# Kernel tuning notes

Hardware: AMD Instinct MI355X
Metric: run time of the kernel (lower is better)

The kernel has to match this reference:

```python
import jax, jax.numpy as jnp
import numpy as np

B, S, E, H = 2, 2048, 512, 8
D = E // H  # head_dim = 64


def setup_inputs() -> dict:
    key = jax.random.key(0)
    ks = jax.random.split(key, 10)
    sc = 1.0 / np.sqrt(E)
    x = jax.random.normal(ks[0], (B, S, E), dtype=jnp.float32)
    # parent index per node: tree_structure[b][parent[b,i]] contains i
    parent = jax.random.randint(ks[1], (B, S), 0, S, dtype=jnp.int32)
    Wp = jax.random.normal(ks[2], (E, E), dtype=jnp.float32) * sc
    bp = jnp.zeros((E,), dtype=jnp.float32)
    Wc = jax.random.normal(ks[3], (E, E), dtype=jnp.float32) * sc
    bc = jnp.zeros((E,), dtype=jnp.float32)
    Ws = jax.random.normal(ks[4], (E, E), dtype=jnp.float32) * sc
    bs = jnp.zeros((E,), dtype=jnp.float32)
    Wo = jax.random.normal(ks[5], (E, E), dtype=jnp.float32) * sc
    bo = jnp.zeros((E,), dtype=jnp.float32)
    return {"x": x, "parent": parent, "Wp": Wp, "bp": bp, "Wc": Wc,
            "bc": bc, "Ws": Ws, "bs": bs, "Wo": Wo, "bo": bo}


def _tree_mask(parent):
    # Vectorized equivalent of the per-batch scatter loop:
    # mask[b, p, c] = mask[b, c, p] = 1 for each (parent, child) edge.
    b_idx = jnp.arange(B)[:, None]
    rows = jnp.arange(S)[None, :]
    m = jnp.zeros((B, S, S), dtype=bool)
    m = m.at[b_idx, rows, parent].set(True)
    m = m.at[b_idx, parent, rows].set(True)
    return m  # (B, S, S), broadcast over heads


def reference(x, parent, Wp, bp, Wc, bc, Ws, bs, Wo, bo):
    # Tri-projection
    p = (x @ Wp + bp).reshape(B, S, H, D)
    c = (x @ Wc + bc).reshape(B, S, H, D)
    s = (x @ Ws + bs).reshape(B, S, H, D)
    scores = jnp.einsum('bnhd,bmhd->bnhm', p, c) / jnp.sqrt(jnp.float32(D))
    mask = _tree_mask(parent)  # (B, S, S)
    scores = jnp.where(mask[:, :, None, :], scores, -jnp.inf)
    attn = jax.nn.softmax(scores, axis=-1)  # dropout is identity (train=False)
    out = jnp.einsum('bnhm,bmhd->bnhd', attn, s).reshape(B, S, E)
    return out @ Wo + bo
```

## Files before the change

kernel.cpp:

```cpp
#include <hip/hip_runtime.h>
#include <hip/hip_bf16.h>

#define B_  2
#define S_  2048
#define E_  512
#define H_  8
#define D_  64
#define BS_ (B_ * S_)
#define N1_ 1536
#define K_  512

typedef __bf16 bf16x8 __attribute__((ext_vector_type(8)));
typedef float  f32x4  __attribute__((ext_vector_type(4)));
typedef unsigned short us8 __attribute__((ext_vector_type(8)));

__device__ __forceinline__ ushort f2bf(float f) {
    unsigned u = __float_as_uint(f);
    unsigned r = (u + 0x7FFFu + ((u >> 16) & 1u)) >> 16;
    return (ushort)r;
}
__device__ __forceinline__ float bf2f(ushort b) {
    return __uint_as_float(((unsigned)b) << 16);
}

__device__ __forceinline__ void gld_lds16(const ushort* g, ushort* l) {
    __builtin_amdgcn_global_load_lds(
        (const __attribute__((address_space(1))) unsigned int*)g,
        (__attribute__((address_space(3))) unsigned int*)l, 16, 0, 0);
}

__global__ __launch_bounds__(256) void prep_kernel(
    const float* __restrict__ Wp, const float* __restrict__ Wc,
    const float* __restrict__ Ws, const float* __restrict__ Wo,
    ushort* __restrict__ Wcat_t, ushort* __restrict__ Wo_t) {
    __shared__ ushort T[64][65];
    int bid2 = blockIdx.x;
    int tid = threadIdx.x;
    int z = bid2 >> 6;
    int t = bid2 & 63;
    const float* src = (z == 0) ? Wp : (z == 1) ? Wc : (z == 2) ? Ws : Wo;
    ushort* dst = (z < 3) ? (Wcat_t + (size_t)z * 512 * 512) : Wo_t;
    int n0 = (t & 7) * 64, k0 = (t >> 3) * 64;
    int g = tid >> 6, l = tid & 63;
    #pragma unroll
    for (int r = 0; r < 16; r++) {
        int kk = g * 16 + r;
        T[kk][l] = f2bf(src[(size_t)(k0 + kk) * 512 + n0 + l]);
    }
    __syncthreads();
    #pragma unroll
    for (int r = 0; r < 16; r++) {
        int nn = g * 16 + r;
        dst[(size_t)(n0 + nn) * 512 + k0 + l] = T[l][nn];
    }
}

template<int TM, int TN, bool BF16OUT, bool A32>
__global__ __launch_bounds__(256) void gemm_mfma_kernel(
    const void* __restrict__ Av,
    const ushort* __restrict__ Bt,
    const float*  __restrict__ b0,
    const float*  __restrict__ b1,
    const float*  __restrict__ b2,
    void* __restrict__ Cv,
    int N, int K) {
    constexpr int TK = 64;
    constexpr int FM = TM / 32;
    constexpr int NF = TN / 32;
    __shared__ ushort As[2][TM][TK];
    __shared__ ushort Bs[2][TN][TK];

    const ushort* Ab = (const ushort*)Av;
    const float*  Af = (const float*)Av;

    const int tid  = threadIdx.x;
    const int lane = tid & 63;
    const int wave = tid >> 6;
    const int wm = wave >> 1, wn = wave & 1;

    const int nbx = gridDim.x;
    const int nwg = gridDim.x * gridDim.y;
    const int lin = blockIdx.y * nbx + blockIdx.x;
    const int swz = (lin & 7) * (nwg >> 3) + (lin >> 3);
    const int row0 = (swz / nbx) * TM;
    const int col0 = (swz % nbx) * TN;

    f32x4 acc[FM][NF] = {};

    const int srow = lane >> 3;
    const int scol = (lane & 7) * 8;

    const int lrow = lane & 15;
    const int lk   = (lane >> 4) * 8;

    const int arow = wave * (TM / 4) + srow;
    const ushort* gab = Ab + (size_t)(row0 + arow) * K + scol;
    const float*  gaf = Af + (size_t)(row0 + arow) * K + scol;
    const ushort* gbb = Bt + (size_t)(col0 + wave * (TN / 4) + srow) * K + scol;

    auto stageB = [&](int buf, int kt) {
        const ushort* gb = gbb + kt;
        #pragma unroll
        for (int j = 0; j < NF; j++)
            gld_lds16(gb + (size_t)j * 8 * K, &Bs[buf][wave * (TN / 4) + j * 8][0]);
    };
    auto stageA_lds = [&](int buf, int kt) {
        const ushort* ga = gab + kt;
        #pragma unroll
        for (int j = 0; j < FM; j++)
            gld_lds16(ga + (size_t)j * 8 * K, &As[buf][wave * (TM / 4) + j * 8][0]);
    };

    f32x4 ar[FM][2];
    auto loadA_regs = [&](int kt) {
        #pragma unroll
        for (int j = 0; j < FM; j++) {
            const float* p = gaf + (size_t)j * 8 * K + kt;
            ar[j][0] = *(const f32x4*)p;
            ar[j][1] = *(const f32x4*)(p + 4);
        }
    };
    auto writeA_lds = [&](int buf) {
        #pragma unroll
        for (int j = 0; j < FM; j++) {
            us8 o;
            #pragma unroll
            for (int q = 0; q < 4; q++) { o[q] = f2bf(ar[j][0][q]); o[q + 4] = f2bf(ar[j][1][q]); }
            *(us8*)(&As[buf][arow + j * 8][scol]) = o;
        }
    };

    if (A32) {
        loadA_regs(0);
        stageB(0, 0);
        writeA_lds(0);
    } else {
        stageA_lds(0, 0);
        stageB(0, 0);
    }
    __syncthreads();

    const int nt = K / TK;
    int cur = 0;
    for (int t = 0; t < nt; t++) {
        if (t + 1 < nt) {
            if (A32) loadA_regs((t + 1) * TK);
            else     stageA_lds(cur ^ 1, (t + 1) * TK);
            stageB(cur ^ 1, (t + 1) * TK);
        }
        #pragma unroll
        for (int kk = 0; kk < TK; kk += 32) {
            bf16x8 af[FM], bfr[NF];
            #pragma unroll
            for (int i = 0; i < FM; i++)
                af[i] = *(const bf16x8*)(&As[cur][wm * (FM * 16) + i * 16 + lrow][kk + lk]);
            #pragma unroll
            for (int j = 0; j < NF; j++)
                bfr[j] = *(const bf16x8*)(&Bs[cur][wn * (TN / 2) + j * 16 + lrow][kk + lk]);
            #pragma unroll
            for (int i = 0; i < FM; i++)
                #pragma unroll
                for (int j = 0; j < NF; j++)
                    acc[i][j] = __builtin_amdgcn_mfma_f32_16x16x32_bf16(
                        af[i], bfr[j], acc[i][j], 0, 0, 0);
        }
        if (A32 && (t + 1 < nt)) writeA_lds(cur ^ 1);
        __syncthreads();
        cur ^= 1;
    }

    const int ccol = lane & 15;
    const int crow = (lane >> 4) * 4;
    #pragma unroll
    for (int j = 0; j < NF; j++) {
        int gcol = col0 + wn * (TN / 2) + j * 16 + ccol;
        float bias = (gcol < 512) ? b0[gcol]
                   : (gcol < 1024) ? b1[gcol - 512] : b2[gcol - 1024];
        #pragma unroll
        for (int i = 0; i < FM; i++) {
            int grow = row0 + wm * (FM * 16) + i * 16 + crow;
            #pragma unroll
            for (int rg = 0; rg < 4; rg++) {
                float v = acc[i][j][rg] + bias;
                if (BF16OUT)
                    ((ushort*)Cv)[(size_t)(grow + rg) * N + gcol] = f2bf(v);
                else
                    ((float*)Cv)[(size_t)(grow + rg) * N + gcol] = v;
            }
        }
    }
}

__global__ __launch_bounds__(256) void attn_gather_kernel(
    const ushort* __restrict__ PCS, const int* __restrict__ parent,
    ushort* __restrict__ attn) {
    constexpr int CAP = 32;
    __shared__ int clist[4][CAP];
    int gtid = blockIdx.x * blockDim.x + threadIdx.x;
    int w    = gtid >> 6;
    int lane = gtid & 63;
    int wv   = (threadIdx.x >> 6);
    int bbase = ((w >> 11) << 11);
    int i  = w & (S_ - 1);
    int rp = bbase + parent[w];

    us8 p8 = *(const us8*)(PCS + (size_t)w * N1_ + lane * 8);
    const ushort* rm = PCS + (size_t)rp * N1_;
    us8 pc8 = *(const us8*)(rm + 512  + lane * 8);
    us8 ps8 = *(const us8*)(rm + 1024 + lane * 8);

    float pnf[8];
    #pragma unroll
    for (int j = 0; j < 8; j++) pnf[j] = bf2f(p8[j]);

    float Z = 0.f, av[8] = {0.f, 0.f, 0.f, 0.f, 0.f, 0.f, 0.f, 0.f};

    int cnt = 0;
    for (int t0 = 0; t0 < S_; t0 += 256) {
        int4 pv = *(const int4*)(parent + bbase + t0 + lane * 4);
        int pc[4] = {pv.x, pv.y, pv.z, pv.w};
        #pragma unroll
        for (int jj = 0; jj < 4; jj++) {
            int c = bbase + t0 + lane * 4 + jj;
            bool mine = (pc[jj] == i) && (c != rp);
            unsigned long long m2 = __ballot(mine);
            if (m2) {
                int nb = __popcll(m2);
                if (cnt + nb <= CAP) {
                    if (mine) {
                        int slot = cnt + __popcll(m2 & ((1ull << lane) - 1ull));
                        clist[wv][slot] = c;
                    }
                    cnt += nb;
                } else {
                    unsigned long long mm = m2;
                    while (mm) {
                        int l = __ffsll(mm) - 1;
                        mm &= mm - 1;
                        int cc = bbase + t0 + l * 4 + jj;
                        const ushort* rc = PCS + (size_t)cc * N1_;
                        us8 c8 = *(const us8*)(rc + 512  + lane * 8);
                        us8 s8 = *(const us8*)(rc + 1024 + lane * 8);
                        float tt = 0.f;
                        #pragma unroll
                        for (int j = 0; j < 8; j++) tt += pnf[j] * bf2f(c8[j]);
                        tt += __shfl_xor(tt, 1); tt += __shfl_xor(tt, 2); tt += __shfl_xor(tt, 4);
                        float e = __expf(tt * 0.125f);
                        Z += e;
                        #pragma unroll
                        for (int j = 0; j < 8; j++) av[j] += e * bf2f(s8[j]);
                    }
                }
            }
        }
    }

    {
        float t = 0.f;
        #pragma unroll
        for (int j = 0; j < 8; j++) t += pnf[j] * bf2f(pc8[j]);
        t += __shfl_xor(t, 1); t += __shfl_xor(t, 2); t += __shfl_xor(t, 4);
        float e = __expf(t * 0.125f);
        Z += e;
        #pragma unroll
        for (int j = 0; j < 8; j++) av[j] += e * bf2f(ps8[j]);
    }

    for (int e = 0; e < cnt; e++) {
        int c = clist[wv][e];
        const ushort* rc = PCS + (size_t)c * N1_;
        us8 c8 = *(const us8*)(rc + 512  + lane * 8);
        us8 s8 = *(const us8*)(rc + 1024 + lane * 8);
        float t = 0.f;
        #pragma unroll
        for (int j = 0; j < 8; j++) t += pnf[j] * bf2f(c8[j]);
        t += __shfl_xor(t, 1); t += __shfl_xor(t, 2); t += __shfl_xor(t, 4);
        float e2 = __expf(t * 0.125f);
        Z += e2;
        #pragma unroll
        for (int j = 0; j < 8; j++) av[j] += e2 * bf2f(s8[j]);
    }

    float rz = 1.0f / Z;
    us8 o8;
    #pragma unroll
    for (int j = 0; j < 8; j++) o8[j] = f2bf(av[j] * rz);
    *(us8*)(attn + (size_t)w * E_ + lane * 8) = o8;
}

extern "C" void kernel_launch(void* const* d_in, const int* in_sizes, int n_in,
                              void* d_out, int out_size, void* d_ws, size_t ws_size,
                              hipStream_t stream) {
    const float* x      = (const float*)d_in[0];
    const int*   parent = (const int*)  d_in[1];
    const float* Wp     = (const float*)d_in[2];
    const float* bp     = (const float*)d_in[3];
    const float* Wc     = (const float*)d_in[4];
    const float* bc     = (const float*)d_in[5];
    const float* Ws     = (const float*)d_in[6];
    const float* bs     = (const float*)d_in[7];
    const float* Wo     = (const float*)d_in[8];
    const float* bo     = (const float*)d_in[9];
    float* out = (float*)d_out;

    char* ws = (char*)d_ws;
    ushort* Wcat_t  = (ushort*)(ws + 0);
    ushort* Wo_t    = (ushort*)(ws + 1572864);
    ushort* PCS_bf  = (ushort*)(ws + 2097152);
    ushort* attn_bf = (ushort*)(ws + 14680064);

    prep_kernel<<<256, 256, 0, stream>>>(Wp, Wc, Ws, Wo, Wcat_t, Wo_t);

    gemm_mfma_kernel<128, 96, true, true>
        <<<dim3(N1_ / 96, BS_ / 128), 256, 0, stream>>>(
        x, Wcat_t, bp, bc, bs, PCS_bf, N1_, K_);

    attn_gather_kernel<<<BS_ * 64 / 256, 256, 0, stream>>>(
        PCS_bf, parent, attn_bf);

    gemm_mfma_kernel<64, 64, false, false>
        <<<dim3(E_ / 64, BS_ / 64), 256, 0, stream>>>(
        attn_bf, Wo_t, bo, bo, bo, out, E_, K_);
}
```

Measured before the change: 116.1 us.

## Fuse tree-attention gather with output projection GEMM in one kernel

Merges the sparse attention gather kernel and the output-projection GEMM into one kernel. Each block computes 16 attention rows into swizzled LDS, then multiplies them by Wo with MFMA while double-buffering Wo tiles. This removes a kernel launch and the round trip of the attention intermediate through global memory. In exchange there are only 256 blocks, each restaging all of Wo, and each wave processes four rows serially, which lowers parallelism in the gather phase.

```diff
diff --git a/kernel.cpp b/kernel.cpp
--- a/kernel.cpp
+++ b/kernel.cpp
@@ -191,101 +191,154 @@
     }
 }
 
-__global__ __launch_bounds__(256) void attn_gather_kernel(
+__global__ __launch_bounds__(256) void attn_gemm2_kernel(
     const ushort* __restrict__ PCS, const int* __restrict__ parent,
-    ushort* __restrict__ attn) {
-    constexpr int CAP = 32;
-    __shared__ int clist[4][CAP];
-    int gtid = blockIdx.x * blockDim.x + threadIdx.x;
-    int w    = gtid >> 6;
-    int lane = gtid & 63;
-    int wv   = (threadIdx.x >> 6);
-    int bbase = ((w >> 11) << 11);
-    int i  = w & (S_ - 1);
-    int rp = bbase + parent[w];
-
-    us8 p8 = *(const us8*)(PCS + (size_t)w * N1_ + lane * 8);
-    const ushort* rm = PCS + (size_t)rp * N1_;
-    us8 pc8 = *(const us8*)(rm + 512  + lane * 8);
-    us8 ps8 = *(const us8*)(rm + 1024 + lane * 8);
-
-    float pnf[8];
-    #pragma unroll
-    for (int j = 0; j < 8; j++) pnf[j] = bf2f(p8[j]);
-
-    float Z = 0.f, av[8] = {0.f, 0.f, 0.f, 0.f, 0.f, 0.f, 0.f, 0.f};
-
-    int cnt = 0;
-    for (int t0 = 0; t0 < S_; t0 += 256) {
-        int4 pv = *(const int4*)(parent + bbase + t0 + lane * 4);
-        int pc[4] = {pv.x, pv.y, pv.z, pv.w};
-        #pragma unroll
-        for (int jj = 0; jj < 4; jj++) {
-            int c = bbase + t0 + lane * 4 + jj;
-            bool mine = (pc[jj] == i) && (c != rp);
-            unsigned long long m2 = __ballot(mine);
-            if (m2) {
-                int nb = __popcll(m2);
-                if (cnt + nb <= CAP) {
-                    if (mine) {
-                        int slot = cnt + __popcll(m2 & ((1ull << lane) - 1ull));
-                        clist[wv][slot] = c;
-                    }
-                    cnt += nb;
-                } else {
-                    unsigned long long mm = m2;
-                    while (mm) {
-                        int l = __ffsll(mm) - 1;
-                        mm &= mm - 1;
-                        int cc = bbase + t0 + l * 4 + jj;
-                        const ushort* rc = PCS + (size_t)cc * N1_;
-                        us8 c8 = *(const us8*)(rc + 512  + lane * 8);
-                        us8 s8 = *(const us8*)(rc + 1024 + lane * 8);
-                        float tt = 0.f;
-                        #pragma unroll
-                        for (int j = 0; j < 8; j++) tt += pnf[j] * bf2f(c8[j]);
-                        tt += __shfl_xor(tt, 1); tt += __shfl_xor(tt, 2); tt += __shfl_xor(tt, 4);
-                        float e = __expf(tt * 0.125f);
-                        Z += e;
-                        #pragma unroll
-                        for (int j = 0; j < 8; j++) av[j] += e * bf2f(s8[j]);
+    const ushort* __restrict__ Wo_t, const float* __restrict__ bo,
+    float* __restrict__ out) {
+    constexpr int CAP = 16;
+    __shared__ ushort As[16][512];
+    __shared__ ushort Bs[2][512][64];
+    __shared__ int clist[4][4][CAP];
+
+    const int tid  = threadIdx.x;
+    const int lane = tid & 63;
+    const int wv   = tid >> 6;
+    const int r0   = blockIdx.x * 16;
+    const int bbase = (r0 >> 11) << 11;
+
+    const int srow = lane >> 3;
+    const int scol = (lane & 7) * 8;
+    auto stageB = [&](int buf, int kt) {
+        #pragma unroll
+        for (int j = 0; j < 16; j++) {
+            const ushort* g = Wo_t + (size_t)(wv * 128 + j * 8 + srow) * K_ + kt + scol;
+            gld_lds16(g, &Bs[buf][wv * 128 + j * 8][0]);
+        }
+    };
+    stageB(0, 0);
+
+    for (int tt = 0; tt < 4; tt++) {
+        int rloc = wv * 4 + tt;
+        int w = r0 + rloc;
+        int i = w & (S_ - 1);
+        int rp = bbase + parent[w];
+
+        us8 p8 = *(const us8*)(PCS + (size_t)w * N1_ + lane * 8);
+        const ushort* rm = PCS + (size_t)rp * N1_;
+        us8 pc8 = *(const us8*)(rm + 512  + lane * 8);
+        us8 ps8 = *(const us8*)(rm + 1024 + lane * 8);
+
+        float pnf[8];
+        #pragma unroll
+        for (int j = 0; j < 8; j++) pnf[j] = bf2f(p8[j]);
+
+        float Z = 0.f, av[8] = {0.f, 0.f, 0.f, 0.f, 0.f, 0.f, 0.f, 0.f};
+
+        int cnt = 0;
+        for (int t0 = 0; t0 < S_; t0 += 256) {
+            int4 pv = *(const int4*)(parent + bbase + t0 + lane * 4);
+            int pc[4] = {pv.x, pv.y, pv.z, pv.w};
+            #pragma unroll
+            for (int jj = 0; jj < 4; jj++) {
+                int c = bbase + t0 + lane * 4 + jj;
+                bool mine = (pc[jj] == i) && (c != rp);
+                unsigned long long m2 = __ballot(mine);
+                if (m2) {
+                    int nb = __popcll(m2);
+                    if (cnt + nb <= CAP) {
+                        if (mine) {
+                            int slot = cnt + __popcll(m2 & ((1ull << lane) - 1ull));
+                            clist[wv][tt][slot] = c;
+                        }
+                        cnt += nb;
+                    } else {
+                        unsigned long long mm = m2;
+                        while (mm) {
+                            int l = __ffsll(mm) - 1;
+                            mm &= mm - 1;
+                            int cc = bbase + t0 + l * 4 + jj;
+                            const ushort* rc = PCS + (size_t)cc * N1_;
+                            us8 c8 = *(const us8*)(rc + 512  + lane * 8);
+                            us8 s8 = *(const us8*)(rc + 1024 + lane * 8);
+                            float ttv = 0.f;
+                            #pragma unroll
+                            for (int j = 0; j < 8; j++) ttv += pnf[j] * bf2f(c8[j]);
+                            ttv += __shfl_xor(ttv, 1); ttv += __shfl_xor(ttv, 2); ttv += __shfl_xor(ttv, 4);
+                            float e = __expf(ttv * 0.125f);
+                            Z += e;
+                            #pragma unroll
+                            for (int j = 0; j < 8; j++) av[j] += e * bf2f(s8[j]);
+                        }
                     }
                 }
             }
         }
-    }
-
-    {
-        float t = 0.f;
-        #pragma unroll
-        for (int j = 0; j < 8; j++) t += pnf[j] * bf2f(pc8[j]);
-        t += __shfl_xor(t, 1); t += __shfl_xor(t, 2); t += __shfl_xor(t, 4);
-        float e = __expf(t * 0.125f);
-        Z += e;
-        #pragma unroll
-        for (int j = 0; j < 8; j++) av[j] += e * bf2f(ps8[j]);
-    }
-
-    for (int e = 0; e < cnt; e++) {
-        int c = clist[wv][e];
-        const ushort* rc = PCS + (size_t)c * N1_;
-        us8 c8 = *(const us8*)(rc + 512  + lane * 8);
-        us8 s8 = *(const us8*)(rc + 1024 + lane * 8);
-        float t = 0.f;
-        #pragma unroll
-        for (int j = 0; j < 8; j++) t += pnf[j] * bf2f(c8[j]);
-        t += __shfl_xor(t, 1); t += __shfl_xor(t, 2); t += __shfl_xor(t, 4);
-        float e2 = __expf(t * 0.125f);
-        Z += e2;
-        #pragma unroll
-        for (int j = 0; j < 8; j++) av[j] += e2 * bf2f(s8[j]);
-    }
-
-    float rz = 1.0f / Z;
-    us8 o8;
+
+        {
+            float t = 0.f;
+            #pragma unroll
+            for (int j = 0; j < 8; j++) t += pnf[j] * bf2f(pc8[j]);
+            t += __shfl_xor(t, 1); t += __shfl_xor(t, 2); t += __shfl_xor(t, 4);
+            float e = __expf(t * 0.125f);
+            Z += e;
+            #pragma unroll
+            for (int j = 0; j < 8; j++) av[j] += e * bf2f(ps8[j]);
+        }
+
+        for (int e = 0; e < cnt; e++) {
+            int c = clist[wv][tt][e];
+            const ushort* rc = PCS + (size_t)c * N1_;
+            us8 c8 = *(const us8*)(rc + 512  + lane * 8);
+            us8 s8 = *(const us8*)(rc + 1024 + lane * 8);
+            float t = 0.f;
+            #pragma unroll
+            for (int j = 0; j < 8; j++) t += pnf[j] * bf2f(c8[j]);
+            t += __shfl_xor(t, 1); t += __shfl_xor(t, 2); t += __shfl_xor(t, 4);
+            float e2 = __expf(t * 0.125f);
+            Z += e2;
+            #pragma unroll
+            for (int j = 0; j < 8; j++) av[j] += e2 * bf2f(s8[j]);
+        }
+
+        float rz = 1.0f / Z;
+        us8 o8;
+        #pragma unroll
+        for (int j = 0; j < 8; j++) o8[j] = f2bf(av[j] * rz);
+        int colw = (lane * 8) ^ ((rloc & 7) << 3);
+        *(us8*)(&As[rloc][colw]) = o8;
+    }
+    __syncthreads();
+
+    f32x4 acc[8] = {};
+    const int lrow = lane & 15;
+    const int lk   = (lane >> 4) * 8;
+    int cur = 0;
+    for (int t = 0; t < 8; t++) {
+        if (t + 1 < 8) stageB(cur ^ 1, (t + 1) * 64);
+        #pragma unroll
+        for (int kk = 0; kk < 64; kk += 32) {
+            int acol = (t * 64 + kk + lk) ^ ((lrow & 7) << 3);
+            bf16x8 af = *(const bf16x8*)(&As[lrow][acol]);
+            #pragma unroll
+            for (int j = 0; j < 8; j++) {
+                bf16x8 bfr = *(const bf16x8*)(&Bs[cur][wv * 128 + j * 16 + lrow][kk + lk]);
+                acc[j] = __builtin_amdgcn_mfma_f32_16x16x32_bf16(af, bfr, acc[j], 0, 0, 0);
+            }
+        }
+        __syncthreads();
+        cur ^= 1;
+    }
+
+    const int ccol = lane & 15;
+    const int crow = (lane >> 4) * 4;
     #pragma unroll
-    for (int j = 0; j < 8; j++) o8[j] = f2bf(av[j] * rz);
-    *(us8*)(attn + (size_t)w * E_ + lane * 8) = o8;
+    for (int j = 0; j < 8; j++) {
+        int gcol = wv * 128 + j * 16 + ccol;
+        float bias = bo[gcol];
+        #pragma unroll
+        for (int rg = 0; rg < 4; rg++)
+            out[(size_t)(r0 + crow + rg) * E_ + gcol] = acc[j][rg] + bias;
+    }
 }
 
 extern "C" void kernel_launch(void* const* d_in, const int* in_sizes, int n_in,
@@ -307,7 +360,6 @@
     ushort* Wcat_t  = (ushort*)(ws + 0);
     ushort* Wo_t    = (ushort*)(ws + 1572864);
     ushort* PCS_bf  = (ushort*)(ws + 2097152);
-    ushort* attn_bf = (ushort*)(ws + 14680064);
 
     prep_kernel<<<256, 256, 0, stream>>>(Wp, Wc, Ws, Wo, Wcat_t, Wo_t);
 
@@ -315,10 +367,5 @@
         <<<dim3(N1_ / 96, BS_ / 128), 256, 0, stream>>>(
         x, Wcat_t, bp, bc, bs, PCS_bf, N1_, K_);
 
-    attn_gather_kernel<<<BS_ * 64 / 256, 256, 0, stream>>>(
-        PCS_bf, parent, attn_bf);
-
-    gemm_mfma_kernel<64, 64, false, false>
-        <<<dim3(E_ / 64, BS_ / 64), 256, 0, stream>>>(
-        attn_bf, Wo_t, bo, bo, bo, out, E_, K_);
-}
+    attn_gemm2_kernel<<<256, 256, 0, stream>>>(PCS_bf, parent, Wo_t, bo, out);
+}
```

Result: slower. 125.6 us (+8.2%).
